# Performance work log

Measured on AMD Instinct MI355X. Metric: run time of the kernel, lower is better.

## Reference

```python
import jax, jax.numpy as jnp
import numpy as np

N = 8192
IN_C = 512
OUT_C = 512


def setup_inputs() -> dict:
    key = jax.random.key(0)
    k1, k2, k3 = jax.random.split(key, 3)
    x = jax.random.normal(k1, (N, IN_C), dtype=jnp.float32)
    adj = jax.random.uniform(k2, (N, N), dtype=jnp.float32)
    # torch.rand initializer for the weight (uniform [0,1))
    w = jax.random.uniform(k3, (IN_C, OUT_C), dtype=jnp.float32)
    return {"x": x, "adj": adj, "w": w}


def reference(x, adj, w):
    # A = adj + I
    A = adj + jnp.eye(adj.shape[0], dtype=adj.dtype)
    # D_hat = diag(deg)^{-1/2}; diagonal inverse + sqrt == elementwise rsqrt of degrees
    deg = jnp.sum(A, axis=1)                      # [N]
    d_inv_sqrt = jax.lax.rsqrt(deg)               # [N]
    # A_hat = D_hat @ A @ D_hat == row/col scaling (same math, no dense inverse)
    A_hat = A * d_inv_sqrt[:, None] * d_inv_sqrt[None, :]
    mm_1 = A_hat @ x                              # [N, in_c]
    return jax.nn.elu(mm_1 @ w)                   # [N, out_c]
```

## Files before the change

### kernel.cpp

```cpp
#include <hip/hip_runtime.h>

#define NN 8192
#define CC 512

typedef __attribute__((ext_vector_type(8))) short short8;
typedef __attribute__((ext_vector_type(4))) float f32x4;
typedef unsigned short ushort_t;

__device__ __forceinline__ unsigned short f2bf(float f) {
    unsigned int u = __float_as_uint(f);
    u += 0x7FFF + ((u >> 16) & 1);
    return (unsigned short)(u >> 16);
}
__device__ __forceinline__ float bf2f(unsigned short u) {
    return __uint_as_float(((unsigned int)u) << 16);
}

__device__ __forceinline__ void gload_lds16(const void* g, void* l) {
    __builtin_amdgcn_global_load_lds((const __attribute__((address_space(1))) unsigned int*)g,
                                     (__attribute__((address_space(3))) unsigned int*)l,
                                     16, 0, 0);
}

__global__ __launch_bounds__(256) void k_rowsum_cvt(const float* __restrict__ adj,
                                                    float* __restrict__ ds,
                                                    ushort_t* __restrict__ adj16) {
    int row = blockIdx.x;
    const float4* p = (const float4*)(adj + (size_t)row * NN);
    ushort4* q = (ushort4*)(adj16 + (size_t)row * NN);
    float s = 0.f;
#pragma unroll
    for (int i = 0; i < 8; ++i) {
        float4 v = p[threadIdx.x + i * 256];
        s += (v.x + v.y) + (v.z + v.w);
        ushort4 u;
        u.x = f2bf(v.x); u.y = f2bf(v.y); u.z = f2bf(v.z); u.w = f2bf(v.w);
        q[threadIdx.x + i * 256] = u;
    }
#pragma unroll
    for (int off = 32; off > 0; off >>= 1) s += __shfl_down(s, off, 64);
    __shared__ float partial[4];
    if ((threadIdx.x & 63) == 0) partial[threadIdx.x >> 6] = s;
    __syncthreads();
    if (threadIdx.x == 0) {
        float deg = ((partial[0] + partial[1]) + (partial[2] + partial[3])) + 1.0f;
        ds[row] = rsqrtf(deg);
    }
}

__global__ __launch_bounds__(256) void k_rowsum(const float* __restrict__ adj,
                                                float* __restrict__ ds) {
    int row = blockIdx.x;
    const float4* p = (const float4*)(adj + (size_t)row * NN);
    float s = 0.f;
#pragma unroll
    for (int i = 0; i < 8; ++i) {
        float4 v = p[threadIdx.x + i * 256];
        s += (v.x + v.y) + (v.z + v.w);
    }
#pragma unroll
    for (int off = 32; off > 0; off >>= 1) s += __shfl_down(s, off, 64);
    __shared__ float partial[4];
    if ((threadIdx.x & 63) == 0) partial[threadIdx.x >> 6] = s;
    __syncthreads();
    if (threadIdx.x == 0) {
        float deg = ((partial[0] + partial[1]) + (partial[2] + partial[3])) + 1.0f;
        ds[row] = rsqrtf(deg);
    }
}

__global__ __launch_bounds__(256) void k_cvt(const float* __restrict__ in,
                                             ushort_t* __restrict__ out) {
    size_t i = (size_t)blockIdx.x * 256 + threadIdx.x;
    float4 v = ((const float4*)in)[i];
    ushort4 u;
    u.x = f2bf(v.x); u.y = f2bf(v.y); u.z = f2bf(v.z); u.w = f2bf(v.w);
    ((ushort4*)out)[i] = u;
}

__global__ __launch_bounds__(256) void k_transpose(const float* __restrict__ in,
                                                   ushort_t* __restrict__ out,
                                                   const float* __restrict__ scale,
                                                   int R, int C) {
    __shared__ float tile[64][65];
    int r0 = blockIdx.x * 64, c0 = blockIdx.y * 64;
    int t = threadIdx.x;
    int cl = t & 63;
    int rl0 = t >> 6;
#pragma unroll
    for (int i = 0; i < 16; ++i) {
        int r = rl0 + i * 4;
        float v = in[(size_t)(r0 + r) * C + c0 + cl];
        float sc = scale ? scale[r0 + r] : 1.0f;
        tile[r][cl] = v * sc;
    }
    __syncthreads();
#pragma unroll
    for (int i = 0; i < 16; ++i) {
        int c = rl0 + i * 4;
        int r = cl;
        out[(size_t)(c0 + c) * R + r0 + r] = f2bf(tile[r][c]);
    }
}

template <bool ELU>
__global__ __launch_bounds__(256, 2) void k_gemm2t(const ushort_t* __restrict__ A,
                                                   const ushort_t* __restrict__ Bt,
                                                   float* __restrict__ out) {
    __shared__ __align__(16) ushort_t As[128 * 64];
    __shared__ __align__(16) ushort_t Bs[128 * 64];

    int t = threadIdx.x;
    int wid = t >> 6, lane = t & 63;
    int bid = blockIdx.x;
    bid = (bid & 7) * 32 + (bid >> 3);
    int cb = bid & 3, rb = bid >> 2;
    int rowBase = rb * 128, colBase = cb * 128;

    int srow0 = t >> 3, ss = t & 7;

    f32x4 acc[4][4] = {};
    int wr = wid >> 1, wc = wid & 1;
    int fr = lane & 15, fq = lane >> 4;

    for (int kt = 0; kt < CC / 64; ++kt) {
#pragma unroll
        for (int j = 0; j < 4; ++j) {
            int row = j * 32 + srow0;
            gload_lds16((const char*)(A + (size_t)(rowBase + row) * CC + kt * 64 +
                                      ((ss ^ (row & 7)) << 3)),
                        (char*)As + j * 4096 + wid * 1024);
            gload_lds16((const char*)(Bt + (size_t)(colBase + row) * CC + kt * 64 +
                                      ((ss ^ (row & 7)) << 3)),
                        (char*)Bs + j * 4096 + wid * 1024);
        }
        __syncthreads();
#pragma unroll
        for (int ks = 0; ks < 2; ++ks) {
            short8 af[4], bf[4];
#pragma unroll
            for (int m = 0; m < 4; ++m) {
                int row = wr * 64 + m * 16 + fr;
                af[m] = *(const short8*)((const char*)As + row * 128 +
                                         ((ks * 64 + fq * 16) ^ ((row & 7) << 4)));
            }
#pragma unroll
            for (int n = 0; n < 4; ++n) {
                int col = wc * 64 + n * 16 + fr;
                bf[n] = *(const short8*)((const char*)Bs + col * 128 +
                                         ((ks * 64 + fq * 16) ^ ((col & 7) << 4)));
            }
#pragma unroll
            for (int m = 0; m < 4; ++m)
#pragma unroll
                for (int n = 0; n < 4; ++n)
                    acc[m][n] = __builtin_amdgcn_mfma_f32_16x16x32_bf16(af[m], bf[n], acc[m][n], 0, 0, 0);
        }
        __syncthreads();
    }

#pragma unroll
    for (int m = 0; m < 4; ++m) {
#pragma unroll
        for (int j = 0; j < 4; ++j) {
            int gr = rowBase + wr * 64 + m * 16 + fq * 4 + j;
#pragma unroll
            for (int n = 0; n < 4; ++n) {
                int gc = colBase + wc * 64 + n * 16 + fr;
                float v = acc[m][n][j];
                out[(size_t)gr * CC + gc] = ELU ? (v > 0.f ? v : expm1f(v)) : v;
            }
        }
    }
}

__global__ __launch_bounds__(512, 1) void k_gemm1d(const ushort_t* __restrict__ adj16,
                                                   const ushort_t* __restrict__ yt2,
                                                   ushort_t* __restrict__ part16) {
    __shared__ __align__(16) ushort_t Al[4][256 * 32];
    __shared__ __align__(16) ushort_t Bl[4][256 * 32];

    int t = threadIdx.x;
    int wid = t >> 6, lane = t & 63;
    int fr = lane & 15, fq = lane >> 4;

    int gid = blockIdx.x;
    int xcd = gid & 7, slot = gid >> 3;
    int cb = slot & 1;
    int u = (slot >> 1) + 16 * xcd;
    int rb = u & 31, ks = u >> 5;
    int rowBase = rb * 256, colBase = cb * 256;
    int kt0 = ks * 64;

    int wr = wid >> 2, wc = wid & 3;
    int bcol0 = (wc & 1) * 64;

    int srow = t >> 2;
    int sw = ((t & 3) ^ ((srow >> 1) & 3)) << 3;
    const ushort_t* aBase = adj16 + (size_t)(rowBase + srow) * NN + sw;
    const ushort_t* bBase = yt2 + (size_t)(colBase + srow) * NN + sw;

    auto stageA = [&](int buf, int tile) {
        gload_lds16(aBase + (size_t)tile * 32, (char*)Al[buf] + wid * 1024);
        gload_lds16(aBase + (size_t)128 * NN + (size_t)tile * 32, (char*)Al[buf] + 8192 + wid * 1024);
    };
    auto stageB = [&](int buf, int tile) {
        gload_lds16(bBase + (size_t)tile * 32, (char*)Bl[buf] + wid * 1024);
        gload_lds16(bBase + (size_t)128 * NN + (size_t)tile * 32, (char*)Bl[buf] + 8192 + wid * 1024);
    };

    f32x4 acc[8][4] = {};
    int sws = (fq ^ ((fr >> 1) & 3)) << 4;

    stageA(0, kt0 + 0); stageB(0, kt0 + 0);
    stageA(1, kt0 + 1); stageB(1, kt0 + 1);
    stageA(2, kt0 + 2); stageB(2, kt0 + 2);
    asm volatile("s_waitcnt vmcnt(8)" ::: "memory");
    __builtin_amdgcn_sched_barrier(0);
    __builtin_amdgcn_s_barrier();

    for (int i = 0; i < 64; ++i) {
        int cur = i & 3;
        int nbuf = (i + 3) & 3;
        int ntile = kt0 + ((i + 3) & 63);
        const char* Ab = (const char*)Al[cur] + wr * 8192;
        const char* Bb = (const char*)Bl[cur] + (wc >> 1) * 8192;

        short8 af0[4], bfv[4];
#pragma unroll
        for (int m = 0; m < 4; ++m)
            af0[m] = *(const short8*)(Ab + (m * 16 + fr) * 64 + sws);
#pragma unroll
        for (int n = 0; n < 4; ++n)
            bfv[n] = *(const short8*)(Bb + (bcol0 + n * 16 + fr) * 64 + sws);
        stageA(nbuf, ntile);
        __builtin_amdgcn_s_barrier();
        __builtin_amdgcn_s_setprio(1);
#pragma unroll
        for (int m = 0; m < 4; ++m)
#pragma unroll
            for (int n = 0; n < 4; ++n)
                acc[m][n] = __builtin_amdgcn_mfma_f32_16x16x32_bf16(af0[m], bfv[n], acc[m][n], 0, 0, 0);
        __builtin_amdgcn_s_setprio(0);
        __builtin_amdgcn_s_barrier();

        short8 af1[4];
#pragma unroll
        for (int m = 0; m < 4; ++m)
            af1[m] = *(const short8*)(Ab + ((64 + m * 16 + fr) * 64) + sws);
        stageB(nbuf, ntile);
        asm volatile("s_waitcnt vmcnt(8)" ::: "memory");
        __builtin_amdgcn_sched_barrier(0);
        __builtin_amdgcn_s_barrier();
        __builtin_amdgcn_s_setprio(1);
#pragma unroll
        for (int m = 0; m < 4; ++m)
#pragma unroll
            for (int n = 0; n < 4; ++n)
                acc[4 + m][n] = __builtin_amdgcn_mfma_f32_16x16x32_bf16(af1[m], bfv[n], acc[4 + m][n], 0, 0, 0);
        __builtin_amdgcn_s_setprio(0);
        __builtin_amdgcn_s_barrier();
    }

#pragma unroll
    for (int m = 0; m < 8; ++m) {
#pragma unroll
        for (int jj = 0; jj < 4; ++jj) {
            int gr = rowBase + wr * 128 + m * 16 + fq * 4 + jj;
            ushort_t* dst = part16 + ((size_t)ks * NN + gr) * CC + colBase;
#pragma unroll
            for (int n = 0; n < 4; ++n)
                dst[wc * 64 + n * 16 + fr] = f2bf(acc[m][n][jj]);
        }
    }
}

__global__ __launch_bounds__(256) void k_finish2(const ushort_t* __restrict__ part16,
                                                 const float* __restrict__ ds,
                                                 const float* __restrict__ z,
                                                 float* __restrict__ out) {
    size_t i = (size_t)blockIdx.x * 256 + threadIdx.x;
    const size_t stride = (size_t)NN * CC / 4;
    float s0 = 0.f, s1 = 0.f, s2 = 0.f, s3 = 0.f;
#pragma unroll
    for (int k = 0; k < 4; ++k) {
        ushort4 p = ((const ushort4*)part16)[i + k * stride];
        s0 += bf2f(p.x); s1 += bf2f(p.y); s2 += bf2f(p.z); s3 += bf2f(p.w);
    }
    int row = (int)(i >> 7);
    float d = ds[row];
    float d2 = d * d;
    f32x4 zv = ((const f32x4*)z)[i];
    f32x4 o;
    float v;
    v = d * s0 + d2 * zv[0]; o[0] = v > 0.f ? v : expm1f(v);
    v = d * s1 + d2 * zv[1]; o[1] = v > 0.f ? v : expm1f(v);
    v = d * s2 + d2 * zv[2]; o[2] = v > 0.f ? v : expm1f(v);
    v = d * s3 + d2 * zv[3]; o[3] = v > 0.f ? v : expm1f(v);
    ((f32x4*)out)[i] = o;
}

__global__ __launch_bounds__(256, 4) void k_gemm1_fb(const float* __restrict__ adj,
                                                     const ushort_t* __restrict__ yt,
                                                     const float* __restrict__ ds,
                                                     const float* __restrict__ x,
                                                     ushort_t* __restrict__ mm1) {
    __shared__ __align__(16) ushort_t As[128 * 64];
    __shared__ __align__(16) ushort_t Bs[128 * 64];

    int t = threadIdx.x;
    int wid = t >> 6, lane = t & 63;
    int bid = blockIdx.x;
    bid = (bid & 7) * 32 + (bid >> 3);
    int colBase = (bid & 3) * 128;
    int rowBase = (bid >> 2) * 128;

    int ar = t >> 4;
    int ac4 = t & 15;
    const float* aptr = adj + (size_t)(rowBase + ar) * NN + ac4 * 4;
    int brow0 = t >> 3;
    int bs = t & 7;
    float4 areg[8];

    auto loadA = [&](int kt) {
        const float* p = aptr + kt * 64;
#pragma unroll
        for (int i = 0; i < 8; ++i)
            areg[i] = *(const float4*)(p + (size_t)i * 16 * NN);
    };
    auto writeA = [&]() {
#pragma unroll
        for (int i = 0; i < 8; ++i) {
            int row = i * 16 + ar;
            ushort4 u;
            u.x = f2bf(areg[i].x); u.y = f2bf(areg[i].y);
            u.z = f2bf(areg[i].z); u.w = f2bf(areg[i].w);
            *(ushort4*)((char*)As + row * 128 + ((ac4 * 8) ^ ((row & 7) << 4))) = u;
        }
    };

    f32x4 acc[4][4] = {};
    int wr = wid >> 1, wc = wid & 1;
    int fr = lane & 15, fq = lane >> 4;

    loadA(0);
    for (int kt = 0; kt < NN / 64; ++kt) {
        writeA();
#pragma unroll
        for (int j = 0; j < 4; ++j) {
            int row = j * 32 + brow0;
            gload_lds16((const char*)(yt + (size_t)(colBase + row) * NN + kt * 64 +
                                      ((bs ^ (row & 7)) << 3)),
                        (char*)Bs + j * 4096 + wid * 1024);
        }
        __syncthreads();
        if (kt + 1 < NN / 64) loadA(kt + 1);
#pragma unroll
        for (int ks2 = 0; ks2 < 2; ++ks2) {
            short8 af[4], bf[4];
#pragma unroll
            for (int m = 0; m < 4; ++m) {
                int row = wr * 64 + m * 16 + fr;
                af[m] = *(const short8*)((const char*)As + row * 128 +
                                         ((ks2 * 64 + fq * 16) ^ ((row & 7) << 4)));
            }
#pragma unroll
            for (int n = 0; n < 4; ++n) {
                int col = wc * 64 + n * 16 + fr;
                bf[n] = *(const short8*)((const char*)Bs + col * 128 +
                                         ((ks2 * 64 + fq * 16) ^ ((col & 7) << 4)));
            }
#pragma unroll
            for (int m = 0; m < 4; ++m)
#pragma unroll
                for (int n = 0; n < 4; ++n)
                    acc[m][n] = __builtin_amdgcn_mfma_f32_16x16x32_bf16(af[m], bf[n], acc[m][n], 0, 0, 0);
        }
        __syncthreads();
    }

#pragma unroll
    for (int m = 0; m < 4; ++m) {
#pragma unroll
        for (int j = 0; j < 4; ++j) {
            int gr = rowBase + wr * 64 + m * 16 + fq * 4 + j;
            float dsr = ds[gr];
#pragma unroll
            for (int n = 0; n < 4; ++n) {
                int gc = colBase + wc * 64 + n * 16 + fr;
                float v = dsr * (acc[m][n][j] + dsr * x[(size_t)gr * CC + gc]);
                mm1[(size_t)gr * CC + gc] = f2bf(v);
            }
        }
    }
}

extern "C" void kernel_launch(void* const* d_in, const int* in_sizes, int n_in,
                              void* d_out, int out_size, void* d_ws, size_t ws_size,
                              hipStream_t stream) {
    const float* x   = (const float*)d_in[0];
    const float* adj = (const float*)d_in[1];
    const float* w   = (const float*)d_in[2];
    float* out = (float*)d_out;

    char* ws = (char*)d_ws;
    size_t off = 0;
    float*    ds  = (float*)(ws + off);  off += 32u << 10;
    ushort_t* yt  = (ushort_t*)(ws + off);  off += 8u << 20;
    ushort_t* wt  = (ushort_t*)(ws + off);  off += 512u << 10;
    ushort_t* xb  = (ushort_t*)(ws + off);  off += 8u << 20;
    float*    z   = (float*)(ws + off);  off += 16u << 20;
    ushort_t* part16 = (ushort_t*)(ws + off);  off += 32u << 20;
    ushort_t* adj16  = (ushort_t*)(ws + off);
    const size_t adjBytes = (size_t)NN * NN * 2;

    if (ws_size >= off + adjBytes) {
        k_rowsum_cvt<<<NN, 256, 0, stream>>>(adj, ds, adj16);
        k_cvt<<<NN * CC / 4 / 256, 256, 0, stream>>>(x, xb);
        k_transpose<<<dim3(CC / 64, CC / 64), 256, 0, stream>>>(w, wt, nullptr, CC, CC);
        k_gemm2t<false><<<256, 256, 0, stream>>>(xb, wt, z);
        k_transpose<<<dim3(NN / 64, CC / 64), 256, 0, stream>>>(z, yt, ds, NN, CC);
        k_gemm1d<<<256, 512, 0, stream>>>(adj16, yt, part16);
        k_finish2<<<NN * CC / 4 / 256, 256, 0, stream>>>(part16, ds, z, out);
    } else {
        ushort_t* mm1 = xb;
        k_rowsum<<<NN, 256, 0, stream>>>(adj, ds);
        k_transpose<<<dim3(NN / 64, CC / 64), 256, 0, stream>>>(x, yt, ds, NN, CC);
        k_transpose<<<dim3(CC / 64, CC / 64), 256, 0, stream>>>(w, wt, nullptr, CC, CC);
        k_gemm1_fb<<<256, 256, 0, stream>>>(adj, yt, ds, x, mm1);
        k_gemm2t<true><<<256, 256, 0, stream>>>(mm1, wt, out);
    }
}
```

Before: 197.2 us.

## Fuse adj rowsum/convert with x@W GEMM and software-pipeline LDS reads in main GEMM

Merges the adjacency row-sum/bf16 conversion, the x-to-bf16 conversion and the x@W GEMM into one launch. The first 256 blocks run the GEMM, converting x to bf16 while staging it into LDS, and the remaining blocks do the row sums. The main adj GEMM now prefetches the next tile's A/B fragments from LDS during the current MFMAs, double-buffering register fragments, and its launch bounds allow 2 blocks per CU. This removes two launches and the xb round-trip and hides LDS latency, at the cost of more register pressure and a larger combined grid.

```diff
diff --git a/kernel.cpp b/kernel.cpp
--- a/kernel.cpp
+++ b/kernel.cpp
@@ -22,20 +22,118 @@
                                      16, 0, 0);
 }
 
-__global__ __launch_bounds__(256) void k_rowsum_cvt(const float* __restrict__ adj,
-                                                    float* __restrict__ ds,
-                                                    ushort_t* __restrict__ adj16) {
+__global__ __launch_bounds__(256) void k_pre(const float* __restrict__ x,
+                                             const float* __restrict__ adj,
+                                             const ushort_t* __restrict__ wt,
+                                             float* __restrict__ ds,
+                                             ushort_t* __restrict__ adj16,
+                                             float* __restrict__ z) {
+    __shared__ __align__(16) ushort_t As[128 * 64];
+    __shared__ __align__(16) ushort_t Bs[128 * 64];
+    __shared__ float partial[4];
+
+    int t = threadIdx.x;
+    if (blockIdx.x >= 256) {
+        int row = blockIdx.x - 256;
+        const float4* p = (const float4*)(adj + (size_t)row * NN);
+        ushort4* q = (ushort4*)(adj16 + (size_t)row * NN);
+        float s = 0.f;
+#pragma unroll
+        for (int i = 0; i < 8; ++i) {
+            float4 v = p[t + i * 256];
+            s += (v.x + v.y) + (v.z + v.w);
+            ushort4 u;
+            u.x = f2bf(v.x); u.y = f2bf(v.y); u.z = f2bf(v.z); u.w = f2bf(v.w);
+            q[t + i * 256] = u;
+        }
+#pragma unroll
+        for (int off = 32; off > 0; off >>= 1) s += __shfl_down(s, off, 64);
+        if ((t & 63) == 0) partial[t >> 6] = s;
+        __syncthreads();
+        if (t == 0) {
+            float deg = ((partial[0] + partial[1]) + (partial[2] + partial[3])) + 1.0f;
+            ds[row] = rsqrtf(deg);
+        }
+        return;
+    }
+
+    int bid = blockIdx.x;
+    int wid = t >> 6, lane = t & 63;
+    int cb = bid & 3, rb = bid >> 2;
+    int rowBase = rb * 128, colBase = cb * 128;
+
+    int ar = t >> 4, ac4 = t & 15;
+    const float* aptr = x + (size_t)(rowBase + ar) * CC + ac4 * 4;
+    int srow0 = t >> 3, ss = t & 7;
+
+    f32x4 acc[4][4] = {};
+    int wr = wid >> 1, wc = wid & 1;
+    int fr = lane & 15, fq = lane >> 4;
+
+    for (int kt = 0; kt < CC / 64; ++kt) {
+#pragma unroll
+        for (int i2 = 0; i2 < 8; ++i2) {
+            float4 v = *(const float4*)(aptr + kt * 64 + (size_t)i2 * 16 * CC);
+            int row = i2 * 16 + ar;
+            ushort4 u2;
+            u2.x = f2bf(v.x); u2.y = f2bf(v.y); u2.z = f2bf(v.z); u2.w = f2bf(v.w);
+            *(ushort4*)((char*)As + row * 128 + ((ac4 * 8) ^ ((row & 7) << 4))) = u2;
+        }
+#pragma unroll
+        for (int j = 0; j < 4; ++j) {
+            int row = j * 32 + srow0;
+            gload_lds16((const char*)(wt + (size_t)(colBase + row) * CC + kt * 64 +
+                                      ((ss ^ (row & 7)) << 3)),
+                        (char*)Bs + j * 4096 + wid * 1024);
+        }
+        __syncthreads();
+#pragma unroll
+        for (int ks = 0; ks < 2; ++ks) {
+            short8 af[4], bfv[4];
+#pragma unroll
+            for (int m = 0; m < 4; ++m) {
+                int row = wr * 64 + m * 16 + fr;
+                af[m] = *(const short8*)((const char*)As + row * 128 +
+                                         ((ks * 64 + fq * 16) ^ ((row & 7) << 4)));
+            }
+#pragma unroll
+            for (int n = 0; n < 4; ++n) {
+                int col = wc * 64 + n * 16 + fr;
+                bfv[n] = *(const short8*)((const char*)Bs + col * 128 +
+                                          ((ks * 64 + fq * 16) ^ ((col & 7) << 4)));
+            }
+#pragma unroll
+            for (int m = 0; m < 4; ++m)
+#pragma unroll
+                for (int n = 0; n < 4; ++n)
+                    acc[m][n] = __builtin_amdgcn_mfma_f32_16x16x32_bf16(af[m], bfv[n], acc[m][n], 0, 0, 0);
+        }
+        __syncthreads();
+    }
+
+#pragma unroll
+    for (int m = 0; m < 4; ++m) {
+#pragma unroll
+        for (int j = 0; j < 4; ++j) {
+            int gr = rowBase + wr * 64 + m * 16 + fq * 4 + j;
+#pragma unroll
+            for (int n = 0; n < 4; ++n) {
+                int gc = colBase + wc * 64 + n * 16 + fr;
+                z[(size_t)gr * CC + gc] = acc[m][n][j];
+            }
+        }
+    }
+}
+
+__global__ __launch_bounds__(256) void k_rowsum(const float* __restrict__ adj,
+                                                float* __restrict__ ds) {
     int row = blockIdx.x;
     const float4* p = (const float4*)(adj + (size_t)row * NN);
-    ushort4* q = (ushort4*)(adj16 + (size_t)row * NN);
     float s = 0.f;
 #pragma unroll
     for (int i = 0; i < 8; ++i) {
         float4 v = p[threadIdx.x + i * 256];
         s += (v.x + v.y) + (v.z + v.w);
-        ushort4 u;
-        u.x = f2bf(v.x); u.y = f2bf(v.y); u.z = f2bf(v.z); u.w = f2bf(v.w);
-        q[threadIdx.x + i * 256] = u;
     }
 #pragma unroll
     for (int off = 32; off > 0; off >>= 1) s += __shfl_down(s, off, 64);
@@ -46,36 +144,6 @@
         float deg = ((partial[0] + partial[1]) + (partial[2] + partial[3])) + 1.0f;
         ds[row] = rsqrtf(deg);
     }
-}
-
-__global__ __launch_bounds__(256) void k_rowsum(const float* __restrict__ adj,
-                                                float* __restrict__ ds) {
-    int row = blockIdx.x;
-    const float4* p = (const float4*)(adj + (size_t)row * NN);
-    float s = 0.f;
-#pragma unroll
-    for (int i = 0; i < 8; ++i) {
-        float4 v = p[threadIdx.x + i * 256];
-        s += (v.x + v.y) + (v.z + v.w);
-    }
-#pragma unroll
-    for (int off = 32; off > 0; off >>= 1) s += __shfl_down(s, off, 64);
-    __shared__ float partial[4];
-    if ((threadIdx.x & 63) == 0) partial[threadIdx.x >> 6] = s;
-    __syncthreads();
-    if (threadIdx.x == 0) {
-        float deg = ((partial[0] + partial[1]) + (partial[2] + partial[3])) + 1.0f;
-        ds[row] = rsqrtf(deg);
-    }
-}
-
-__global__ __launch_bounds__(256) void k_cvt(const float* __restrict__ in,
-                                             ushort_t* __restrict__ out) {
-    size_t i = (size_t)blockIdx.x * 256 + threadIdx.x;
-    float4 v = ((const float4*)in)[i];
-    ushort4 u;
-    u.x = f2bf(v.x); u.y = f2bf(v.y); u.z = f2bf(v.z); u.w = f2bf(v.w);
-    ((ushort4*)out)[i] = u;
 }
 
 __global__ __launch_bounds__(256) void k_transpose(const float* __restrict__ in,
@@ -137,7 +205,7 @@
         __syncthreads();
 #pragma unroll
         for (int ks = 0; ks < 2; ++ks) {
-            short8 af[4], bf[4];
+            short8 af[4], bfv[4];
 #pragma unroll
             for (int m = 0; m < 4; ++m) {
                 int row = wr * 64 + m * 16 + fr;
@@ -147,14 +215,14 @@
 #pragma unroll
             for (int n = 0; n < 4; ++n) {
                 int col = wc * 64 + n * 16 + fr;
-                bf[n] = *(const short8*)((const char*)Bs + col * 128 +
-                                         ((ks * 64 + fq * 16) ^ ((col & 7) << 4)));
+                bfv[n] = *(const short8*)((const char*)Bs + col * 128 +
+                                          ((ks * 64 + fq * 16) ^ ((col & 7) << 4)));
             }
 #pragma unroll
             for (int m = 0; m < 4; ++m)
 #pragma unroll
                 for (int n = 0; n < 4; ++n)
-                    acc[m][n] = __builtin_amdgcn_mfma_f32_16x16x32_bf16(af[m], bf[n], acc[m][n], 0, 0, 0);
+                    acc[m][n] = __builtin_amdgcn_mfma_f32_16x16x32_bf16(af[m], bfv[n], acc[m][n], 0, 0, 0);
         }
         __syncthreads();
     }
@@ -174,7 +242,7 @@
     }
 }
 
-__global__ __launch_bounds__(512, 1) void k_gemm1d(const ushort_t* __restrict__ adj16,
+__global__ __launch_bounds__(512, 2) void k_gemm1d(const ushort_t* __restrict__ adj16,
                                                    const ushort_t* __restrict__ yt2,
                                                    ushort_t* __restrict__ part16) {
     __shared__ __align__(16) ushort_t Al[4][256 * 32];
@@ -212,6 +280,54 @@
     f32x4 acc[8][4] = {};
     int sws = (fq ^ ((fr >> 1) & 3)) << 4;
 
+    auto readA0 = [&](short8 (&d)[4], int buf) {
+        const char* Ab = (const char*)Al[buf] + wr * 8192;
+#pragma unroll
+        for (int m = 0; m < 4; ++m) d[m] = *(const short8*)(Ab + (m * 16 + fr) * 64 + sws);
+    };
+    auto readA1 = [&](short8 (&d)[4], int buf) {
+        const char* Ab = (const char*)Al[buf] + wr * 8192;
+#pragma unroll
+        for (int m = 0; m < 4; ++m) d[m] = *(const short8*)(Ab + (64 + m * 16 + fr) * 64 + sws);
+    };
+    auto readB = [&](short8 (&d)[4], int buf) {
+        const char* Bb = (const char*)Bl[buf] + (wc >> 1) * 8192;
+#pragma unroll
+        for (int n = 0; n < 4; ++n) d[n] = *(const short8*)(Bb + (bcol0 + n * 16 + fr) * 64 + sws);
+    };
+
+    auto iter = [&](int i, short8 (&cf0)[4], short8 (&cbf)[4],
+                    short8 (&nf0)[4], short8 (&nbf)[4]) {
+        int nbuf = (i + 3) & 3;
+        int ntile = kt0 + ((i + 3) & 63);
+        short8 af1[4];
+        readA1(af1, i & 3);
+        stageA(nbuf, ntile);
+        __builtin_amdgcn_s_barrier();
+        __builtin_amdgcn_s_setprio(1);
+#pragma unroll
+        for (int m = 0; m < 4; ++m)
+#pragma unroll
+            for (int n = 0; n < 4; ++n)
+                acc[m][n] = __builtin_amdgcn_mfma_f32_16x16x32_bf16(cf0[m], cbf[n], acc[m][n], 0, 0, 0);
+        __builtin_amdgcn_s_setprio(0);
+        __builtin_amdgcn_s_barrier();
+        stageB(nbuf, ntile);
+        asm volatile("s_waitcnt vmcnt(8)" ::: "memory");
+        __builtin_amdgcn_sched_barrier(0);
+        __builtin_amdgcn_s_barrier();
+        readA0(nf0, (i + 1) & 3);
+        readB(nbf, (i + 1) & 3);
+        __builtin_amdgcn_s_setprio(1);
+#pragma unroll
+        for (int m = 0; m < 4; ++m)
+#pragma unroll
+            for (int n = 0; n < 4; ++n)
+                acc[4 + m][n] = __builtin_amdgcn_mfma_f32_16x16x32_bf16(af1[m], cbf[n], acc[4 + m][n], 0, 0, 0);
+        __builtin_amdgcn_s_setprio(0);
+        __builtin_amdgcn_s_barrier();
+    };
+
     stageA(0, kt0 + 0); stageB(0, kt0 + 0);
     stageA(1, kt0 + 1); stageB(1, kt0 + 1);
     stageA(2, kt0 + 2); stageB(2, kt0 + 2);
@@ -219,47 +335,13 @@
     __builtin_amdgcn_sched_barrier(0);
     __builtin_amdgcn_s_barrier();
 
-    for (int i = 0; i < 64; ++i) {
-        int cur = i & 3;
-        int nbuf = (i + 3) & 3;
-        int ntile = kt0 + ((i + 3) & 63);
-        const char* Ab = (const char*)Al[cur] + wr * 8192;
-        const char* Bb = (const char*)Bl[cur] + (wc >> 1) * 8192;
-
-        short8 af0[4], bfv[4];
-#pragma unroll
-        for (int m = 0; m < 4; ++m)
-            af0[m] = *(const short8*)(Ab + (m * 16 + fr) * 64 + sws);
-#pragma unroll
-        for (int n = 0; n < 4; ++n)
-            bfv[n] = *(const short8*)(Bb + (bcol0 + n * 16 + fr) * 64 + sws);
-        stageA(nbuf, ntile);
-        __builtin_amdgcn_s_barrier();
-        __builtin_amdgcn_s_setprio(1);
-#pragma unroll
-        for (int m = 0; m < 4; ++m)
-#pragma unroll
-            for (int n = 0; n < 4; ++n)
-                acc[m][n] = __builtin_amdgcn_mfma_f32_16x16x32_bf16(af0[m], bfv[n], acc[m][n], 0, 0, 0);
-        __builtin_amdgcn_s_setprio(0);
-        __builtin_amdgcn_s_barrier();
-
-        short8 af1[4];
-#pragma unroll
-        for (int m = 0; m < 4; ++m)
-            af1[m] = *(const short8*)(Ab + ((64 + m * 16 + fr) * 64) + sws);
-        stageB(nbuf, ntile);
-        asm volatile("s_waitcnt vmcnt(8)" ::: "memory");
-        __builtin_amdgcn_sched_barrier(0);
-        __builtin_amdgcn_s_barrier();
-        __builtin_amdgcn_s_setprio(1);
-#pragma unroll
-        for (int m = 0; m < 4; ++m)
-#pragma unroll
-            for (int n = 0; n < 4; ++n)
-                acc[4 + m][n] = __builtin_amdgcn_mfma_f32_16x16x32_bf16(af1[m], bfv[n], acc[4 + m][n], 0, 0, 0);
-        __builtin_amdgcn_s_setprio(0);
-        __builtin_amdgcn_s_barrier();
+    short8 pf0[4], pbf[4], qf0[4], qbf[4];
+    readA0(pf0, 0);
+    readB(pbf, 0);
+
+    for (int ii = 0; ii < 32; ++ii) {
+        iter(2 * ii,     pf0, pbf, qf0, qbf);
+        iter(2 * ii + 1, qf0, qbf, pf0, pbf);
     }
 
 #pragma unroll
@@ -357,7 +439,7 @@
         if (kt + 1 < NN / 64) loadA(kt + 1);
 #pragma unroll
         for (int ks2 = 0; ks2 < 2; ++ks2) {
-            short8 af[4], bf[4];
+            short8 af[4], bfv[4];
 #pragma unroll
             for (int m = 0; m < 4; ++m) {
                 int row = wr * 64 + m * 16 + fr;
@@ -367,14 +449,14 @@
 #pragma unroll
             for (int n = 0; n < 4; ++n) {
                 int col = wc * 64 + n * 16 + fr;
-                bf[n] = *(const short8*)((const char*)Bs + col * 128 +
-                                         ((ks2 * 64 + fq * 16) ^ ((col & 7) << 4)));
+                bfv[n] = *(const short8*)((const char*)Bs + col * 128 +
+                                          ((ks2 * 64 + fq * 16) ^ ((col & 7) << 4)));
             }
 #pragma unroll
             for (int m = 0; m < 4; ++m)
 #pragma unroll
                 for (int n = 0; n < 4; ++n)
-                    acc[m][n] = __builtin_amdgcn_mfma_f32_16x16x32_bf16(af[m], bf[n], acc[m][n], 0, 0, 0);
+                    acc[m][n] = __builtin_amdgcn_mfma_f32_16x16x32_bf16(af[m], bfv[n], acc[m][n], 0, 0, 0);
         }
         __syncthreads();
     }
@@ -415,10 +497,8 @@
     const size_t adjBytes = (size_t)NN * NN * 2;
 
     if (ws_size >= off + adjBytes) {
-        k_rowsum_cvt<<<NN, 256, 0, stream>>>(adj, ds, adj16);
-        k_cvt<<<NN * CC / 4 / 256, 256, 0, stream>>>(x, xb);
         k_transpose<<<dim3(CC / 64, CC / 64), 256, 0, stream>>>(w, wt, nullptr, CC, CC);
-        k_gemm2t<false><<<256, 256, 0, stream>>>(xb, wt, z);
+        k_pre<<<NN + 256, 256, 0, stream>>>(x, adj, wt, ds, adj16, z);
         k_transpose<<<dim3(NN / 64, CC / 64), 256, 0, stream>>>(z, yt, ds, NN, CC);
         k_gemm1d<<<256, 512, 0, stream>>>(adj16, yt, part16);
         k_finish2<<<NN * CC / 4 / 256, 256, 0, stream>>>(part16, ds, z, out);
```

After: 196.8 us. No clear change (-0.2%).
